# Optimization experiments

Measured on AMD Instinct MI355X. Metric: run time of the kernel, lower is better.

Reference implementation:

```python
import jax, jax.numpy as jnp
import numpy as np

U = 256  # units


def _lstm_scan(x, W, R, bc):
    """Run the custom LSTM over time axis of x [B,T,D].

    W: (D,4U) stacked [ki|kf|ko|kc]; R: (U,4U) stacked [ri|rf|ro|rc]; bc: (U,).
    Faithful quirks: no bias on i/f/o gates; c_new = sigmoid(f*c + i*cand);
    h_new = tanh(c_new) * o.
    Returns (last_h [B,U], outputs [B,T,U]).
    """
    B = x.shape[0]
    xW = jnp.einsum('btd,dg->tbg', x, W)  # precompute input projections, (T,B,4U)

    def step(carry, xw):
        h, c = carry
        g = xw + h @ R  # (B,4U)
        i = jax.nn.sigmoid(g[:, 0 * U:1 * U])
        f = jax.nn.sigmoid(g[:, 1 * U:2 * U])
        o = jax.nn.sigmoid(g[:, 2 * U:3 * U])
        cand = jnp.tanh(g[:, 3 * U:4 * U] + bc)
        c_new = jax.nn.sigmoid(f * c + i * cand)
        h_new = jnp.tanh(c_new) * o
        return (h_new, c_new), h_new

    h0 = jnp.zeros((B, U), dtype=x.dtype)
    c0 = jnp.zeros((B, U), dtype=x.dtype)
    (h_last, _), hs = jax.lax.scan(step, (h0, c0), xW)
    return h_last, jnp.swapaxes(hs, 0, 1)  # (B,T,U)


def setup_inputs() -> dict:
    key = jax.random.key(0)
    ks = jax.random.split(key, 5)
    B, T, D = 16, 2048, 256
    s_in = 1.0 / np.sqrt(D)
    s_rec = 1.0 / np.sqrt(U)
    return {
        'x': jax.random.normal(ks[0], (B, T, D), dtype=jnp.float32),
        'W_f': jax.random.normal(ks[1], (D, 4 * U), dtype=jnp.float32) * s_in,
        'R_f': jax.random.normal(ks[2], (U, 4 * U), dtype=jnp.float32) * s_rec,
        'bc_f': jnp.zeros((U,), dtype=jnp.float32),
        'W_b': jax.random.normal(ks[3], (D, 4 * U), dtype=jnp.float32) * s_in,
        'R_b': jax.random.normal(ks[4], (U, 4 * U), dtype=jnp.float32) * s_rec,
        'bc_b': jnp.zeros((U,), dtype=jnp.float32),
    }


def reference(x, W_f, R_f, bc_f, W_b, R_b, bc_b):
    # forward direction
    _, out_f = _lstm_scan(x, W_f, R_f, bc_f)
    # backward direction: K.rnn(go_backwards=True) iterates reversed inputs and
    # returns outputs in iteration (reversed-time) order, NOT re-reversed.
    _, out_b = _lstm_scan(x[:, ::-1, :], W_b, R_b, bc_b)
    return jnp.concatenate([out_f, out_b], axis=-1)  # (B,T,2U)
```

## Files before the change

### kernel.cpp

```cpp
#include <hip/hip_runtime.h>
#include <hip/hip_bf16.h>
#include <hip/hip_fp16.h>

#define TT 2048
#define BB 16
#define DD 256
#define GG 1024
#define UU 256

using f32x4  = __attribute__((ext_vector_type(4))) float;
using short8 = __attribute__((ext_vector_type(8))) short;
using f16x8  = __attribute__((ext_vector_type(8))) _Float16;
using u32x4  = __attribute__((ext_vector_type(4))) unsigned int;

static __device__ __forceinline__ unsigned short f2h_u(float f){
  _Float16 h = (_Float16)f;
  return __builtin_bit_cast(unsigned short, h);
}
static __device__ __forceinline__ float h2f(unsigned short u){
  return (float)__builtin_bit_cast(_Float16, u);
}
static __device__ __forceinline__ unsigned short f2bf_u(float f){
  __hip_bfloat16 b = __float2bfloat16(f);
  return __builtin_bit_cast(unsigned short, b);
}
static __device__ __forceinline__ float sigmoid_f(float x){
  return 1.0f / (1.0f + __expf(-x));
}
static __device__ __forceinline__ float tanh_f(float x){
  float ax = fabsf(x);
  float e  = __expf(2.0f*ax);
  float r  = 1.0f - 2.0f/(e + 1.0f);
  return copysignf(r, x);
}
static __device__ __forceinline__ f32x4 mfma16x16x32_f16(f16x8 a, f16x8 b, f32x4 c){
  return __builtin_amdgcn_mfma_f32_16x16x32_f16(a, b, c, 0, 0, 0);
}
static __device__ __forceinline__ void lds_barrier(){
  __builtin_amdgcn_sched_barrier(0);
  asm volatile("s_waitcnt lgkmcnt(0)" ::: "memory");
  __builtin_amdgcn_s_barrier();
  __builtin_amdgcn_sched_barrier(0);
}

__global__ __launch_bounds__(256) void cvt_x_kernel(const float* __restrict__ x,
                                                    unsigned short* __restrict__ xh){
  int gid = blockIdx.x*256 + threadIdx.x;
  const float4* xv = (const float4*)x;
  float4 v = xv[gid];
  unsigned int u0 = (unsigned int)f2bf_u(v.x) | ((unsigned int)f2bf_u(v.y) << 16);
  unsigned int u1 = (unsigned int)f2bf_u(v.z) | ((unsigned int)f2bf_u(v.w) << 16);
  ((uint2*)xh)[gid] = make_uint2(u0, u1);
}

__global__ __launch_bounds__(256) void cvt_wt_kernel(const float* __restrict__ Wf,
                                                     const float* __restrict__ Wb,
                                                     unsigned short* __restrict__ wt){
  int gid = blockIdx.x*256 + threadIdx.x;
  int d   = gid >> 18;
  int rem = gid & 262143;
  int n   = rem >> 8;
  int k   = rem & 255;
  const float* src = d ? Wb : Wf;
  wt[gid] = f2bf_u(src[k*GG + n]);
}

__global__ __launch_bounds__(256) void cvt_rt_kernel(const float* __restrict__ Rf,
                                                     const float* __restrict__ Rb,
                                                     unsigned short* __restrict__ rt){
  int gid = blockIdx.x*256 + threadIdx.x;
  int d   = gid >> 18;
  int rem = gid & 262143;
  int c   = rem >> 8;
  int p   = rem & 255;
  int Qb  = c >> 7, tc = c & 127;
  int ul  = tc >> 2, g = tc & 3;
  int ucol = g*256 + Qb*32 + ul;
  int s = p >> 5, l4g = (p >> 3) & 3, e = p & 7;
  int k = 32*s + (e < 4 ? 4*l4g + e : 16 + 4*l4g + (e - 4));
  const float* src = d ? Rb : Rf;
  rt[gid] = f2h_u(src[k*GG + ucol]);
}

__global__ __launch_bounds__(256) void gemm_projT(const unsigned short* __restrict__ Ah,
                                                  const unsigned short* __restrict__ BTh,
                                                  unsigned short* __restrict__ Cd,
                                                  int xstart, int Tc){
  __shared__ __align__(16) unsigned short smem[18432];
  unsigned short* sA = smem;
  unsigned short* sB = smem + 9216;
  unsigned short* sC = smem;

  int mt  = blockIdx.x >> 3;
  int nt  = blockIdx.x & 7;
  int tid = threadIdx.x;

  const unsigned short* Bb = BTh + (size_t)nt*128*DD;

  int w = tid >> 6, lane = tid & 63, l15 = lane & 15, l4 = lane >> 4;
  int wm = w >> 1, wn = w & 1;

  f32x4 zero4 = {0.0f, 0.0f, 0.0f, 0.0f};
  f32x4 acc[4][4];
#pragma unroll
  for (int i = 0; i < 4; ++i)
#pragma unroll
    for (int j = 0; j < 4; ++j) acc[i][j] = zero4;

  for (int kt = 0; kt < 4; ++kt){
    __syncthreads();
#pragma unroll
    for (int i = 0; i < 4; ++i){
      int ch = tid + i*256;
      int r = ch >> 3, c8 = ch & 7;
      int bb = r >> 3, ti = r & 7;
      int tx = xstart + mt*8 + ti;
      *(uint4*)(sA + r*72 + c8*8) = *(const uint4*)(Ah + ((size_t)bb*TT + tx)*DD + kt*64 + c8*8);
      *(uint4*)(sB + r*72 + c8*8) = *(const uint4*)(Bb + (size_t)r*DD + kt*64 + c8*8);
    }
    __syncthreads();
#pragma unroll
    for (int ks = 0; ks < 2; ++ks){
      short8 a[4], b[4];
#pragma unroll
      for (int mf = 0; mf < 4; ++mf)
        a[mf] = *(const short8*)(sA + (wm*64 + mf*16 + l15)*72 + ks*32 + l4*8);
#pragma unroll
      for (int nf = 0; nf < 4; ++nf)
        b[nf] = *(const short8*)(sB + (wn*64 + nf*16 + l15)*72 + ks*32 + l4*8);
#pragma unroll
      for (int mf = 0; mf < 4; ++mf)
#pragma unroll
        for (int nf = 0; nf < 4; ++nf)
          acc[mf][nf] = __builtin_amdgcn_mfma_f32_16x16x32_bf16(a[mf], b[nf], acc[mf][nf], 0, 0, 0);
    }
  }
  __syncthreads();
#pragma unroll
  for (int mf = 0; mf < 4; ++mf)
#pragma unroll
    for (int nf = 0; nf < 4; ++nf)
#pragma unroll
      for (int r = 0; r < 4; ++r)
        sC[(wm*64 + mf*16 + l4*4 + r)*136 + wn*64 + nf*16 + l15] = f2h_u(acc[mf][nf][r]);
  __syncthreads();
  int c = tid >> 1, half = tid & 1;
#pragma unroll
  for (int ti = 0; ti < 8; ++ti){
    unsigned short* slab = Cd + ((size_t)(mt*8 + ti)*GG + nt*128)*16;
    unsigned short v[8];
#pragma unroll
    for (int j = 0; j < 8; ++j)
      v[j] = sC[((half*8 + j)*8 + ti)*136 + c];
    uint4 pk;
    pk.x = (unsigned int)v[0] | ((unsigned int)v[1] << 16);
    pk.y = (unsigned int)v[2] | ((unsigned int)v[3] << 16);
    pk.z = (unsigned int)v[4] | ((unsigned int)v[5] << 16);
    pk.w = (unsigned int)v[6] | ((unsigned int)v[7] << 16);
    *(uint4*)(slab + c*16 + half*8) = pk;
  }
}

template<int Q>
__device__ __forceinline__ void scan_body(
    unsigned short* hT,
    const unsigned short* __restrict__ projT,
    const unsigned short* __restrict__ rt,
    const float* __restrict__ bcf, const float* __restrict__ bcb,
    float* __restrict__ out,
    float* __restrict__ stH, float* __restrict__ stC,
    unsigned short* __restrict__ xchg,
    int* __restrict__ flags,
    int t0, int t1, int Tc, int first, int d)
{
  int tid = threadIdx.x;
  int w = tid >> 6, l = tid & 63, l15 = l & 15, l4 = l >> 4;

  u32x4 frag[8];
  {
    const unsigned short* Rd = rt + (size_t)d*262144
                             + ((size_t)(Q*128 + w*16 + l15))*256 + l4*8;
#pragma unroll
    for (int s = 0; s < 8; ++s)
      frag[s] = *(const u32x4*)(Rd + s*32);
  }
#pragma unroll
  for (int s = 0; s < 8; ++s)
    asm volatile("" : "+v"(frag[s]));

  const float* stHb = stH + d*4096;
  for (int idx = tid; idx < 4096; idx += 512){
    int b = idx >> 8, u = idx & 255;
    hT[(u >> 2)*68 + b*4 + (u & 3)] = first ? (unsigned short)0
                                            : f2h_u(stHb[b*256 + u]);
  }

  const int u_loc = 4*w + l4, u_g = 32*Q + u_loc;
  float c_r = 0.f, h_r = 0.f;
  if (!first) c_r = stC[(d*16 + l15)*256 + u_g];
  float bc_r = (d ? bcb : bcf)[u_g];

  const unsigned short* prj = projT + (size_t)d*Tc*16384;
  const int myflag = (d*8 + Q)*32;
  const int p = (Q + w) & 7;
  const int paflag = (d*8 + p)*32;
  const unsigned long long* xull = (const unsigned long long*)xchg;
  const int Tl = t1 - t0;

  __syncthreads();

  for (int s = 0; s < Tl; ++s){
    int t = t0 + s;
    int ps = d ? (Tl - 1 - s) : s;

    const unsigned short* pr = prj + (size_t)ps*16384;
    unsigned short pj0 = pr[(0*256 + u_g)*16 + l15];
    unsigned short pj1 = pr[(1*256 + u_g)*16 + l15];
    unsigned short pj2 = pr[(2*256 + u_g)*16 + l15];
    unsigned short pj3 = pr[(3*256 + u_g)*16 + l15];

    unsigned long long v0 = 0, v1 = 0;
    if (s > 0 && w >= 1){
      while (__hip_atomic_load(&flags[paflag], __ATOMIC_RELAXED, __HIP_MEMORY_SCOPE_AGENT) < s)
        __builtin_amdgcn_s_sleep(1);
      size_t base = (((size_t)d*2 + ((s - 1) & 1))*8 + p)*128;
      v0 = __hip_atomic_load(&xull[base + 2*l    ], __ATOMIC_RELAXED, __HIP_MEMORY_SCOPE_AGENT);
      v1 = __hip_atomic_load(&xull[base + 2*l + 1], __ATOMIC_RELAXED, __HIP_MEMORY_SCOPE_AGENT);
    }

    f32x4 acc = {0.f, 0.f, 0.f, 0.f};
    {
      uint2 b0 = *(const uint2*)&hT[(Q*8     + l4)*68 + l15*4];
      uint2 b1 = *(const uint2*)&hT[(Q*8 + 4 + l4)*68 + l15*4];
      u32x4 bv = {b0.x, b0.y, b1.x, b1.y};
      acc = mfma16x16x32_f16(__builtin_bit_cast(f16x8, frag[Q]),
                             __builtin_bit_cast(f16x8, bv), acc);
    }

    if (s > 0 && w >= 1){
      int uq = 8*p + (l >> 3), bq = 2*(l & 7);
      *(uint2*)&hT[uq*68 + bq*4    ] = make_uint2((unsigned)v0, (unsigned)(v0 >> 32));
      *(uint2*)&hT[uq*68 + bq*4 + 4] = make_uint2((unsigned)v1, (unsigned)(v1 >> 32));
    }
    lds_barrier();

#pragma unroll
    for (int j = 1; j < 8; ++j){
      const int sg = (Q + j) & 7;
      uint2 b0 = *(const uint2*)&hT[(sg*8     + l4)*68 + l15*4];
      uint2 b1 = *(const uint2*)&hT[(sg*8 + 4 + l4)*68 + l15*4];
      u32x4 bv = {b0.x, b0.y, b1.x, b1.y};
      acc = mfma16x16x32_f16(__builtin_bit_cast(f16x8, frag[sg]),
                             __builtin_bit_cast(f16x8, bv), acc);
    }
    lds_barrier();

    float gi = acc[0] + h2f(pj0);
    float gf = acc[1] + h2f(pj1);
    float go = acc[2] + h2f(pj2);
    float gc = acc[3] + h2f(pj3) + bc_r;
    float ig = sigmoid_f(gi);
    float fg = sigmoid_f(gf);
    float og = sigmoid_f(go);
    float cand = tanh_f(gc);
    c_r = sigmoid_f(fg*c_r + ig*cand);
    float h = tanh_f(c_r) * og;
    h_r = h;

    unsigned short hu = f2h_u(h);
    hT[(8*Q + w)*68 + l15*4 + l4] = hu;
    xchg[((size_t)(d*2 + (s & 1))*8 + Q)*512 + w*64 + l15*4 + l4] = hu;
    __builtin_amdgcn_sched_barrier(0);
    out[((size_t)l15*TT + t)*512 + d*256 + u_g] = h;
    __builtin_amdgcn_sched_barrier(0);
    asm volatile("s_waitcnt vmcnt(1) lgkmcnt(0)" ::: "memory");
    __builtin_amdgcn_s_barrier();
    __builtin_amdgcn_sched_barrier(0);
    if (tid == 0)
      __hip_atomic_store(&flags[myflag], s + 1, __ATOMIC_RELAXED, __HIP_MEMORY_SCOPE_AGENT);
  }

  stC[(d*16 + l15)*256 + u_g] = c_r;
  stH[(d*16 + l15)*256 + u_g] = h_r;
}

__global__ __attribute__((amdgpu_flat_work_group_size(512, 512), amdgpu_waves_per_eu(2, 2)))
void lstm_scan_mfma(const unsigned short* __restrict__ projT,
                    const unsigned short* __restrict__ rt,
                    const float* __restrict__ bcf, const float* __restrict__ bcb,
                    float* __restrict__ out,
                    float* __restrict__ stH, float* __restrict__ stC,
                    unsigned short* __restrict__ xchg,
                    int* __restrict__ flags,
                    int t0, int t1, int Tc, int first)
{
  __shared__ __align__(16) unsigned short hT[64*68];
  int blk = blockIdx.x;
  int d = blk & 7, Q = blk >> 3;
  if (d >= 2) return;
  switch (Q){
    case 0: scan_body<0>(hT, projT, rt, bcf, bcb, out, stH, stC, xchg, flags, t0, t1, Tc, first, d); break;
    case 1: scan_body<1>(hT, projT, rt, bcf, bcb, out, stH, stC, xchg, flags, t0, t1, Tc, first, d); break;
    case 2: scan_body<2>(hT, projT, rt, bcf, bcb, out, stH, stC, xchg, flags, t0, t1, Tc, first, d); break;
    case 3: scan_body<3>(hT, projT, rt, bcf, bcb, out, stH, stC, xchg, flags, t0, t1, Tc, first, d); break;
    case 4: scan_body<4>(hT, projT, rt, bcf, bcb, out, stH, stC, xchg, flags, t0, t1, Tc, first, d); break;
    case 5: scan_body<5>(hT, projT, rt, bcf, bcb, out, stH, stC, xchg, flags, t0, t1, Tc, first, d); break;
    case 6: scan_body<6>(hT, projT, rt, bcf, bcb, out, stH, stC, xchg, flags, t0, t1, Tc, first, d); break;
    default: scan_body<7>(hT, projT, rt, bcf, bcb, out, stH, stC, xchg, flags, t0, t1, Tc, first, d); break;
  }
}

extern "C" void kernel_launch(void* const* d_in, const int* in_sizes, int n_in,
                              void* d_out, int out_size, void* d_ws, size_t ws_size,
                              hipStream_t stream){
  const float* x   = (const float*)d_in[0];
  const float* Wf  = (const float*)d_in[1];
  const float* Rf  = (const float*)d_in[2];
  const float* bcf = (const float*)d_in[3];
  const float* Wb  = (const float*)d_in[4];
  const float* Rb  = (const float*)d_in[5];
  const float* bcb = (const float*)d_in[6];
  float* out = (float*)d_out;
  char* ws = (char*)d_ws;

  const size_t OFF_XH    = 0;
  const size_t OFF_WT    = 16777216;
  const size_t OFF_RT    = OFF_WT + 1048576;
  const size_t OFF_STH   = OFF_RT + 1048576;
  const size_t OFF_STC   = OFF_STH + 32768;
  const size_t OFF_XCHG  = OFF_STC + 32768;
  const size_t OFF_FLAGS = OFF_XCHG + 32768;
  const size_t OFF_PROJT = OFF_FLAGS + 4096;

  unsigned short* xh    = (unsigned short*)(ws + OFF_XH);
  unsigned short* wt    = (unsigned short*)(ws + OFF_WT);
  unsigned short* rt    = (unsigned short*)(ws + OFF_RT);
  float*          stH   = (float*)(ws + OFF_STH);
  float*          stC   = (float*)(ws + OFF_STC);
  unsigned short* xchg  = (unsigned short*)(ws + OFF_XCHG);
  int*            flags = (int*)(ws + OFF_FLAGS);
  unsigned short* projT = (unsigned short*)(ws + OFF_PROJT);

  int Tc = TT;
  while (Tc > 128 && OFF_PROJT + (size_t)65536*Tc > ws_size) Tc >>= 1;

  cvt_x_kernel<<<8192, 256, 0, stream>>>(x, xh);
  cvt_wt_kernel<<<2048, 256, 0, stream>>>(Wf, Wb, wt);
  cvt_rt_kernel<<<2048, 256, 0, stream>>>(Rf, Rb, rt);

  int nch = TT / Tc;
  for (int ch = 0; ch < nch; ++ch){
    int t0 = ch*Tc, t1 = t0 + Tc;
    gemm_projT<<<Tc, 256, 0, stream>>>(xh, wt,          projT,                     t0,      Tc);
    gemm_projT<<<Tc, 256, 0, stream>>>(xh, wt + 262144, projT + (size_t)Tc*GG*16,  TT - t1, Tc);
    hipMemsetAsync(flags, 0, 2048, stream);
    lstm_scan_mfma<<<64, 512, 0, stream>>>(projT, rt, bcf, bcb, out, stH, stC, xchg, flags,
                                           t0, t1, Tc, ch == 0 ? 1 : 0);
  }
}
```

Baseline: 3.552 ms.

## Halve scan workgroup to 4 waves, each computing two MFMA tiles per step

The recurrent scan block shrinks from 8 waves to 4, and each wave now holds two sets of R fragments and runs two MFMA chains, so it updates two hidden units per lane. The recurrent weight permutation, the hT LDS layout (contiguous 8-element slabs, one 128-bit load per fragment) and the cross-block exchange are reworked so each wave pulls one or two peer slabs. The second LDS barrier per step is removed, and outputs and state are stored as float2. The aim is to cut barrier and wave synchronisation cost per timestep, at the price of doubled register pressure per wave, longer serial MFMA chains and a much larger LDS allocation.

```diff
diff --git a/kernel.cpp b/kernel.cpp
--- a/kernel.cpp
+++ b/kernel.cpp
@@ -73,13 +73,12 @@
   int rem = gid & 262143;
   int c   = rem >> 8;
   int p   = rem & 255;
-  int Qb  = c >> 7, tc = c & 127;
-  int ul  = tc >> 2, g = tc & 3;
-  int ucol = g*256 + Qb*32 + ul;
-  int s = p >> 5, l4g = (p >> 3) & 3, e = p & 7;
-  int k = 32*s + (e < 4 ? 4*l4g + e : 16 + 4*l4g + (e - 4));
+  int Qb  = c >> 7, ml = c & 127;
+  int w   = ml >> 5, tile = (ml >> 4) & 1, l4c = (ml >> 2) & 3, g = ml & 3;
+  int u_loc = w*8 + 2*l4c + tile;
+  int ucol  = g*256 + Qb*32 + u_loc;
   const float* src = d ? Rb : Rf;
-  rt[gid] = f2h_u(src[k*GG + ucol]);
+  rt[gid] = f2h_u(src[p*GG + ucol]);
 }
 
 __global__ __launch_bounds__(256) void gemm_projT(const unsigned short* __restrict__ Ah,
@@ -176,34 +175,43 @@
   int tid = threadIdx.x;
   int w = tid >> 6, l = tid & 63, l15 = l & 15, l4 = l >> 4;
 
-  u32x4 frag[8];
+  u32x4 fragA[8], fragB[8];
   {
-    const unsigned short* Rd = rt + (size_t)d*262144
-                             + ((size_t)(Q*128 + w*16 + l15))*256 + l4*8;
-#pragma unroll
-    for (int s = 0; s < 8; ++s)
-      frag[s] = *(const u32x4*)(Rd + s*32);
-  }
-#pragma unroll
-  for (int s = 0; s < 8; ++s)
-    asm volatile("" : "+v"(frag[s]));
+    const unsigned short* c0 = rt + (size_t)d*262144
+                             + (size_t)(Q*128 + w*32 + l15)*256 + l4*8;
+#pragma unroll
+    for (int s = 0; s < 8; ++s){
+      fragA[s] = *(const u32x4*)(c0 + s*32);
+      fragB[s] = *(const u32x4*)(c0 + 4096 + s*32);
+    }
+  }
+#pragma unroll
+  for (int s = 0; s < 8; ++s){
+    asm volatile("" : "+v"(fragA[s]));
+    asm volatile("" : "+v"(fragB[s]));
+  }
 
   const float* stHb = stH + d*4096;
-  for (int idx = tid; idx < 4096; idx += 512){
+  for (int idx = tid; idx < 4096; idx += 256){
     int b = idx >> 8, u = idx & 255;
-    hT[(u >> 2)*68 + b*4 + (u & 3)] = first ? (unsigned short)0
-                                            : f2h_u(stHb[b*256 + u]);
-  }
-
-  const int u_loc = 4*w + l4, u_g = 32*Q + u_loc;
-  float c_r = 0.f, h_r = 0.f;
-  if (!first) c_r = stC[(d*16 + l15)*256 + u_g];
-  float bc_r = (d ? bcb : bcf)[u_g];
+    hT[(u >> 3)*128 + b*8 + (u & 7)] = first ? (unsigned short)0
+                                             : f2h_u(stHb[b*256 + u]);
+  }
+
+  const int u0 = 32*Q + w*8 + 2*l4;
+  float c0s = 0.f, c1s = 0.f, h0r = 0.f, h1r = 0.f;
+  if (!first){
+    c0s = stC[(d*16 + l15)*256 + u0];
+    c1s = stC[(d*16 + l15)*256 + u0 + 1];
+  }
+  const float* bc = d ? bcb : bcf;
+  float bc0 = bc[u0], bc1 = bc[u0 + 1];
 
   const unsigned short* prj = projT + (size_t)d*Tc*16384;
   const int myflag = (d*8 + Q)*32;
-  const int p = (Q + w) & 7;
-  const int paflag = (d*8 + p)*32;
+  const int j0 = 2*w + 1;
+  const int p0 = (Q + j0) & 7, p1 = (Q + j0 + 1) & 7;
+  const int pf0 = (d*8 + p0)*32, pf1 = (d*8 + p1)*32;
   const unsigned long long* xull = (const unsigned long long*)xchg;
   const int Tl = t1 - t0;
 
@@ -214,64 +222,79 @@
     int ps = d ? (Tl - 1 - s) : s;
 
     const unsigned short* pr = prj + (size_t)ps*16384;
-    unsigned short pj0 = pr[(0*256 + u_g)*16 + l15];
-    unsigned short pj1 = pr[(1*256 + u_g)*16 + l15];
-    unsigned short pj2 = pr[(2*256 + u_g)*16 + l15];
-    unsigned short pj3 = pr[(3*256 + u_g)*16 + l15];
-
-    unsigned long long v0 = 0, v1 = 0;
-    if (s > 0 && w >= 1){
-      while (__hip_atomic_load(&flags[paflag], __ATOMIC_RELAXED, __HIP_MEMORY_SCOPE_AGENT) < s)
+    unsigned short pj[8];
+#pragma unroll
+    for (int g = 0; g < 4; ++g){
+      pj[g]     = pr[(g*256 + u0    )*16 + l15];
+      pj[4 + g] = pr[(g*256 + u0 + 1)*16 + l15];
+    }
+
+    f32x4 acc0 = {0.f,0.f,0.f,0.f}, acc1 = acc0;
+    {
+      u32x4 bv = *(const u32x4*)&hT[(Q*4 + l4)*128 + l15*8];
+      acc0 = mfma16x16x32_f16(__builtin_bit_cast(f16x8, fragA[Q]),
+                              __builtin_bit_cast(f16x8, bv), acc0);
+      acc1 = mfma16x16x32_f16(__builtin_bit_cast(f16x8, fragB[Q]),
+                              __builtin_bit_cast(f16x8, bv), acc1);
+    }
+
+    if (s > 0){
+      while (__hip_atomic_load(&flags[pf0], __ATOMIC_RELAXED, __HIP_MEMORY_SCOPE_AGENT) < s)
         __builtin_amdgcn_s_sleep(1);
-      size_t base = (((size_t)d*2 + ((s - 1) & 1))*8 + p)*128;
-      v0 = __hip_atomic_load(&xull[base + 2*l    ], __ATOMIC_RELAXED, __HIP_MEMORY_SCOPE_AGENT);
-      v1 = __hip_atomic_load(&xull[base + 2*l + 1], __ATOMIC_RELAXED, __HIP_MEMORY_SCOPE_AGENT);
-    }
-
-    f32x4 acc = {0.f, 0.f, 0.f, 0.f};
-    {
-      uint2 b0 = *(const uint2*)&hT[(Q*8     + l4)*68 + l15*4];
-      uint2 b1 = *(const uint2*)&hT[(Q*8 + 4 + l4)*68 + l15*4];
-      u32x4 bv = {b0.x, b0.y, b1.x, b1.y};
-      acc = mfma16x16x32_f16(__builtin_bit_cast(f16x8, frag[Q]),
-                             __builtin_bit_cast(f16x8, bv), acc);
-    }
-
-    if (s > 0 && w >= 1){
-      int uq = 8*p + (l >> 3), bq = 2*(l & 7);
-      *(uint2*)&hT[uq*68 + bq*4    ] = make_uint2((unsigned)v0, (unsigned)(v0 >> 32));
-      *(uint2*)&hT[uq*68 + bq*4 + 4] = make_uint2((unsigned)v1, (unsigned)(v1 >> 32));
+      size_t sb = ((size_t)d*2 + ((s - 1) & 1))*8;
+      size_t b0 = (sb + p0)*128;
+      unsigned long long v0 = __hip_atomic_load(&xull[b0 + 2*l    ], __ATOMIC_RELAXED, __HIP_MEMORY_SCOPE_AGENT);
+      unsigned long long v1 = __hip_atomic_load(&xull[b0 + 2*l + 1], __ATOMIC_RELAXED, __HIP_MEMORY_SCOPE_AGENT);
+      unsigned long long v2 = 0, v3 = 0;
+      if (w < 3){
+        while (__hip_atomic_load(&flags[pf1], __ATOMIC_RELAXED, __HIP_MEMORY_SCOPE_AGENT) < s)
+          __builtin_amdgcn_s_sleep(1);
+        size_t b1 = (sb + p1)*128;
+        v2 = __hip_atomic_load(&xull[b1 + 2*l    ], __ATOMIC_RELAXED, __HIP_MEMORY_SCOPE_AGENT);
+        v3 = __hip_atomic_load(&xull[b1 + 2*l + 1], __ATOMIC_RELAXED, __HIP_MEMORY_SCOPE_AGENT);
+      }
+      *(uint4*)&hT[p0*512 + l*8] = make_uint4((unsigned)v0, (unsigned)(v0 >> 32),
+                                              (unsigned)v1, (unsigned)(v1 >> 32));
+      if (w < 3)
+        *(uint4*)&hT[p1*512 + l*8] = make_uint4((unsigned)v2, (unsigned)(v2 >> 32),
+                                                (unsigned)v3, (unsigned)(v3 >> 32));
     }
     lds_barrier();
 
 #pragma unroll
     for (int j = 1; j < 8; ++j){
       const int sg = (Q + j) & 7;
-      uint2 b0 = *(const uint2*)&hT[(sg*8     + l4)*68 + l15*4];
-      uint2 b1 = *(const uint2*)&hT[(sg*8 + 4 + l4)*68 + l15*4];
-      u32x4 bv = {b0.x, b0.y, b1.x, b1.y};
-      acc = mfma16x16x32_f16(__builtin_bit_cast(f16x8, frag[sg]),
-                             __builtin_bit_cast(f16x8, bv), acc);
-    }
-    lds_barrier();
-
-    float gi = acc[0] + h2f(pj0);
-    float gf = acc[1] + h2f(pj1);
-    float go = acc[2] + h2f(pj2);
-    float gc = acc[3] + h2f(pj3) + bc_r;
-    float ig = sigmoid_f(gi);
-    float fg = sigmoid_f(gf);
-    float og = sigmoid_f(go);
-    float cand = tanh_f(gc);
-    c_r = sigmoid_f(fg*c_r + ig*cand);
-    float h = tanh_f(c_r) * og;
-    h_r = h;
-
-    unsigned short hu = f2h_u(h);
-    hT[(8*Q + w)*68 + l15*4 + l4] = hu;
-    xchg[((size_t)(d*2 + (s & 1))*8 + Q)*512 + w*64 + l15*4 + l4] = hu;
+      u32x4 bv = *(const u32x4*)&hT[(sg*4 + l4)*128 + l15*8];
+      acc0 = mfma16x16x32_f16(__builtin_bit_cast(f16x8, fragA[sg]),
+                              __builtin_bit_cast(f16x8, bv), acc0);
+      acc1 = mfma16x16x32_f16(__builtin_bit_cast(f16x8, fragB[sg]),
+                              __builtin_bit_cast(f16x8, bv), acc1);
+    }
+
+    float gi0 = acc0[0] + h2f(pj[0]);
+    float gf0 = acc0[1] + h2f(pj[1]);
+    float go0 = acc0[2] + h2f(pj[2]);
+    float gc0 = acc0[3] + h2f(pj[3]) + bc0;
+    float gi1 = acc1[0] + h2f(pj[4]);
+    float gf1 = acc1[1] + h2f(pj[5]);
+    float go1 = acc1[2] + h2f(pj[6]);
+    float gc1 = acc1[3] + h2f(pj[7]) + bc1;
+    float ig0 = sigmoid_f(gi0), fg0 = sigmoid_f(gf0), og0 = sigmoid_f(go0);
+    float ig1 = sigmoid_f(gi1), fg1 = sigmoid_f(gf1), og1 = sigmoid_f(go1);
+    float cd0 = tanh_f(gc0), cd1 = tanh_f(gc1);
+    c0s = sigmoid_f(fg0*c0s + ig0*cd0);
+    c1s = sigmoid_f(fg1*c1s + ig1*cd1);
+    float h0 = tanh_f(c0s) * og0;
+    float h1 = tanh_f(c1s) * og1;
+    h0r = h0; h1r = h1;
+
+    unsigned short hu0 = f2h_u(h0), hu1 = f2h_u(h1);
+    unsigned int hw = (unsigned int)hu0 | ((unsigned int)hu1 << 16);
+    int slabpos = w*128 + l15*8 + 2*l4;
+    *(unsigned int*)&hT[Q*512 + slabpos] = hw;
+    *(unsigned int*)&xchg[((size_t)(d*2 + (s & 1))*8 + Q)*512 + slabpos] = hw;
     __builtin_amdgcn_sched_barrier(0);
-    out[((size_t)l15*TT + t)*512 + d*256 + u_g] = h;
+    *(float2*)&out[((size_t)l15*TT + t)*512 + d*256 + u0] = make_float2(h0, h1);
     __builtin_amdgcn_sched_barrier(0);
     asm volatile("s_waitcnt vmcnt(1) lgkmcnt(0)" ::: "memory");
     __builtin_amdgcn_s_barrier();
@@ -280,11 +303,11 @@
       __hip_atomic_store(&flags[myflag], s + 1, __ATOMIC_RELAXED, __HIP_MEMORY_SCOPE_AGENT);
   }
 
-  stC[(d*16 + l15)*256 + u_g] = c_r;
-  stH[(d*16 + l15)*256 + u_g] = h_r;
-}
-
-__global__ __attribute__((amdgpu_flat_work_group_size(512, 512), amdgpu_waves_per_eu(2, 2)))
+  *(float2*)&stC[(d*16 + l15)*256 + u0] = make_float2(c0s, c1s);
+  *(float2*)&stH[(d*16 + l15)*256 + u0] = make_float2(h0r, h1r);
+}
+
+__global__ __attribute__((amdgpu_flat_work_group_size(256, 256), amdgpu_waves_per_eu(1, 1)))
 void lstm_scan_mfma(const unsigned short* __restrict__ projT,
                     const unsigned short* __restrict__ rt,
                     const float* __restrict__ bcf, const float* __restrict__ bcb,
@@ -294,7 +317,7 @@
                     int* __restrict__ flags,
                     int t0, int t1, int Tc, int first)
 {
-  __shared__ __align__(16) unsigned short hT[64*68];
+  __shared__ __align__(16) unsigned short hT[40960];
   int blk = blockIdx.x;
   int d = blk & 7, Q = blk >> 3;
   if (d >= 2) return;
@@ -354,7 +377,7 @@
     gemm_projT<<<Tc, 256, 0, stream>>>(xh, wt,          projT,                     t0,      Tc);
     gemm_projT<<<Tc, 256, 0, stream>>>(xh, wt + 262144, projT + (size_t)Tc*GG*16,  TT - t1, Tc);
     hipMemsetAsync(flags, 0, 2048, stream);
-    lstm_scan_mfma<<<64, 512, 0, stream>>>(projT, rt, bcf, bcb, out, stH, stC, xchg, flags,
+    lstm_scan_mfma<<<64, 256, 0, stream>>>(projT, rt, bcf, bcb, out, stH, stC, xchg, flags,
                                            t0, t1, Tc, ch == 0 ? 1 : 0);
   }
 }
```

After: 3.490 ms. No clear change (-1.7%).
